# Performance work log

Measured on AMD Instinct MI355X. Metric: run time of the kernel, lower is better.

Reference implementation:

```python
import jax, jax.numpy as jnp
import numpy as np

N_NODES = 100000
N_EDGES = 3200000
IN_DIM = 128
HID = 64


def _gcn_conv(x, src, dst, norm, W, b, n_nodes):
    # x: [N, Fin]; PyG GCNConv: h = x @ W^T, propagate with sym norm, + bias
    h = x @ W.T                                  # [N, Fout]
    msg = h[src] * norm[:, None]                 # gather + scale, [E', Fout]
    out = jax.ops.segment_sum(msg, dst, num_segments=n_nodes)  # scatter-add
    return out + b


def _build_norm(edge_index, n_nodes):
    # add self-loops, compute D^-1/2 A D^-1/2 edge weights
    loops = jnp.arange(n_nodes, dtype=edge_index.dtype)
    src = jnp.concatenate([edge_index[0], loops])
    dst = jnp.concatenate([edge_index[1], loops])
    deg = jax.ops.segment_sum(jnp.ones_like(dst, dtype=jnp.float32), dst,
                              num_segments=n_nodes)
    dinv = jnp.where(deg > 0, jax.lax.rsqrt(jnp.maximum(deg, 1.0)), 0.0)
    norm = dinv[src] * dinv[dst]
    return src, dst, norm


def setup_inputs() -> dict:
    key = jax.random.key(0)
    k = jax.random.split(key, 8)
    x = jax.random.normal(k[0], (N_NODES, IN_DIM), dtype=jnp.float32)
    edge_index = jax.random.randint(k[1], (2, N_EDGES), 0, N_NODES, dtype=jnp.int64)
    s1 = 1.0 / np.sqrt(IN_DIM)
    s2 = 1.0 / np.sqrt(HID)
    W1 = jax.random.uniform(k[2], (HID, IN_DIM), jnp.float32, -s1, s1)
    b1 = jnp.zeros((HID,), jnp.float32)
    W2 = jax.random.uniform(k[3], (HID, HID), jnp.float32, -s2, s2)
    b2 = jnp.zeros((HID,), jnp.float32)
    Wc = jax.random.uniform(k[4], (1, HID), jnp.float32, -s2, s2)
    bc = jax.random.uniform(k[5], (1,), jnp.float32, -s2, s2)
    return {"x": x, "edge_index": edge_index, "W1": W1, "b1": b1,
            "W2": W2, "b2": b2, "Wc": Wc, "bc": bc}


def reference(x, edge_index, W1, b1, W2, b2, Wc, bc):
    n = x.shape[0]
    src, dst, norm = _build_norm(edge_index, n)
    h = _gcn_conv(x, src, dst, norm, W1, b1, n)
    h = jax.nn.relu(h)
    h = _gcn_conv(h, src, dst, norm, W2, b2, n)
    return h @ Wc.T + bc                          # [N, 1]
```

## Files before the change

### kernel.cpp

```cpp
#include <hip/hip_runtime.h>
#include <hip/hip_bf16.h>
#include <hip/hip_fp16.h>

#define N_NODES 100000
#define N_EDGES 3200000
#define F_IN    128
#define F_H     64

#define NBUCK 256
#define NPB   391
#define SRC_BITS 17

#define BH_T 256
#define BH_C 16384
__global__ __launch_bounds__(BH_T) void k_bhist(const int* __restrict__ dst,
                                                int* __restrict__ bcount) {
    __shared__ int lc[NBUCK];
    int t = threadIdx.x;
    lc[t] = 0;
    __syncthreads();
    long long e0 = (long long)blockIdx.x * BH_C;
    long long e1 = e0 + BH_C; if (e1 > N_EDGES) e1 = N_EDGES;
    for (long long e = e0 + t; e < e1; e += BH_T)
        atomicAdd(&lc[dst[e] / NPB], 1);
    __syncthreads();
    int c = lc[t];
    if (c) atomicAdd(&bcount[t], c);
}

__global__ __launch_bounds__(NBUCK) void k_bscan(const int* __restrict__ bcount,
                                                 int* __restrict__ bbase,
                                                 int* __restrict__ bcur,
                                                 int* __restrict__ row_ptr) {
    __shared__ int s[NBUCK];
    int t = threadIdx.x;
    int c = bcount[t];
    s[t] = c;
    __syncthreads();
    for (int off = 1; off < NBUCK; off <<= 1) {
        int v = (t >= off) ? s[t - off] : 0;
        __syncthreads();
        s[t] += v;
        __syncthreads();
    }
    int ex = s[t] - c;
    bbase[t] = ex;
    bcur[t]  = ex;
    if (t == NBUCK - 1) {
        bbase[NBUCK] = s[t];
        row_ptr[N_NODES] = s[t];
    }
}

__global__ __launch_bounds__(64) void k_wc2(const float* __restrict__ W2,
                                            const float* __restrict__ Wc,
                                            const float* __restrict__ b2,
                                            const float* __restrict__ bc,
                                            float* __restrict__ wc2,
                                            float* __restrict__ c0) {
    int k = threadIdx.x;
    float s = 0.0f;
#pragma unroll 8
    for (int f = 0; f < F_H; f++) s += Wc[f] * W2[f * F_H + k];
    wc2[k] = s;
    float p = Wc[k] * b2[k];
#pragma unroll
    for (int off = 32; off > 0; off >>= 1) p += __shfl_xor(p, off, 64);
    if (k == 0) c0[0] = p + bc[0];
}

#define PA_T   256
#define PA_C   4096
#define PA_PER (PA_C / PA_T)
__global__ __launch_bounds__(PA_T) void k_partA(const int* __restrict__ src,
                                                const int* __restrict__ dst,
                                                int* __restrict__ bucket_cursor,
                                                int* __restrict__ packT) {
    __shared__ int lcount[NBUCK];
    __shared__ int lstart[NBUCK];
    __shared__ int loffs[NBUCK];
    __shared__ int lbase[NBUCK];
    __shared__ int s_pack[PA_C];
    __shared__ unsigned char s_bkt[PA_C];
    __shared__ int ltot;
    int t = threadIdx.x;
    long long e0 = (long long)blockIdx.x * PA_C;
    if (t < NBUCK) lcount[t] = 0;
    __syncthreads();
    int ep[PA_PER];
    short eb[PA_PER];
#pragma unroll
    for (int i = 0; i < PA_PER; i++) {
        long long e = e0 + i * PA_T + t;
        if (e < N_EDGES) {
            int es = src[e], ed = dst[e];
            int b = ed / NPB;
            eb[i] = (short)b;
            ep[i] = ((ed - b * NPB) << SRC_BITS) | es;
            atomicAdd(&lcount[b], 1);
        } else eb[i] = -1;
    }
    __syncthreads();
    if (t < 64) {
        int base = t * 4;
        int c0 = lcount[base], c1 = lcount[base + 1], c2 = lcount[base + 2], c3 = lcount[base + 3];
        int ssum = c0 + c1 + c2 + c3;
        int sc = ssum;
#pragma unroll
        for (int off = 1; off < 64; off <<= 1) {
            int v = __shfl_up(sc, off, 64);
            if (t >= off) sc += v;
        }
        int ex = sc - ssum;
        lstart[base]     = ex;
        lstart[base + 1] = ex + c0;
        lstart[base + 2] = ex + c0 + c1;
        lstart[base + 3] = ex + c0 + c1 + c2;
        if (t == 63) ltot = sc;
    }
    __syncthreads();
    if (t < NBUCK) {
        loffs[t] = lstart[t];
        int c = lcount[t];
        lbase[t] = c ? atomicAdd(&bucket_cursor[t], c) : 0;
    }
    __syncthreads();
#pragma unroll
    for (int i = 0; i < PA_PER; i++) {
        if (eb[i] >= 0) {
            int idx = atomicAdd(&loffs[eb[i]], 1);
            s_pack[idx] = ep[i];
            s_bkt[idx] = (unsigned char)eb[i];
        }
    }
    __syncthreads();
    int tot = ltot;
    for (int i = t; i < tot; i += PA_T) {
        int b = s_bkt[i];
        int addr = lbase[b] + (i - lstart[b]);
        packT[addr] = s_pack[i];
    }
}

#define PB_T   1024
#define PB_CAP 16384
__global__ __launch_bounds__(PB_T) void k_partB(const int* __restrict__ bbase,
                                                const int* __restrict__ packT,
                                                int* __restrict__ row_ptr,
                                                float* __restrict__ dinv,
                                                int* __restrict__ srcs) {
    __shared__ int lhist[NPB];
    __shared__ int lcur[NPB];
    __shared__ int s_out[PB_CAP];
    int b = blockIdx.x;
    int node0 = b * NPB;
    int node1 = min(node0 + NPB, N_NODES);
    int nloc = node1 - node0;
    int beg = bbase[b];
    int end = bbase[b + 1];
    int len = end - beg;
    int t = threadIdx.x;
    const int SMASK = (1 << SRC_BITS) - 1;

    for (int i = t; i < NPB; i += PB_T) lhist[i] = 0;
    __syncthreads();
    for (int i = t; i < len; i += PB_T)
        atomicAdd(&lhist[packT[beg + i] >> SRC_BITS], 1);
    __syncthreads();
    if (t < 64) {
        int base = t * 7;
        int c[7]; int ssum = 0;
#pragma unroll
        for (int j = 0; j < 7; j++) {
            int idx = base + j;
            c[j] = (idx < NPB) ? lhist[idx] : 0;
            ssum += c[j];
        }
        int sc = ssum;
#pragma unroll
        for (int off = 1; off < 64; off <<= 1) {
            int v = __shfl_up(sc, off, 64);
            if (t >= off) sc += v;
        }
        int ex = sc - ssum;
#pragma unroll
        for (int j = 0; j < 7; j++) {
            int idx = base + j;
            if (idx < NPB) lcur[idx] = ex;
            ex += c[j];
        }
    }
    __syncthreads();
    for (int i = t; i < nloc; i += PB_T) {
        row_ptr[node0 + i] = beg + lcur[i];
        dinv[node0 + i] = rsqrtf((float)(lhist[i] + 1));
    }
    __syncthreads();
    if (len <= PB_CAP) {
        for (int i = t; i < len; i += PB_T) {
            int pk = packT[beg + i];
            int idx = atomicAdd(&lcur[pk >> SRC_BITS], 1);
            s_out[idx] = pk & SMASK;
        }
        __syncthreads();
        for (int i = t; i < len; i += PB_T)
            srcs[beg + i] = s_out[i];
    } else {
        for (int i = t; i < len; i += PB_T) {
            int pk = packT[beg + i];
            int idx = atomicAdd(&lcur[pk >> SRC_BITS], 1);
            srcs[beg + idx] = pk & SMASK;
        }
    }
}

#define GT   256
#define NTB  128
#define KT   64
#define WTS  68

__global__ __launch_bounds__(GT) void k_gemm1(const float* __restrict__ x,
                                              const float* __restrict__ W1,
                                              const float* __restrict__ dinv,
                                              __half* __restrict__ hs) {
    __shared__ float wT[KT * WTS];
    __shared__ float xT[KT * NTB];
    int t = threadIdx.x;
    int node0 = blockIdx.x * NTB;
    int lane = t & 63, wv = t >> 6;
    int fi = lane & 15, ni = lane >> 4;
    int n0 = wv * 32 + ni * 8;

    float acc[4][8];
#pragma unroll
    for (int r = 0; r < 4; r++)
#pragma unroll
        for (int c = 0; c < 8; c++) acc[r][c] = 0.0f;

    for (int p = 0; p < 2; p++) {
        int k0 = p * KT;
        if (p) __syncthreads();
        {
            int f = t & 63, kq = t >> 6;
            const float4* wp = (const float4*)&W1[(size_t)f * F_IN + k0 + kq * 16];
#pragma unroll
            for (int j = 0; j < 4; j++) {
                float4 v = wp[j];
                int kl = kq * 16 + 4 * j;
                wT[(kl + 0) * WTS + f] = v.x;
                wT[(kl + 1) * WTS + f] = v.y;
                wT[(kl + 2) * WTS + f] = v.z;
                wT[(kl + 3) * WTS + f] = v.w;
            }
        }
        {
            int n = t & 127, half = t >> 7;
            int node = node0 + n;
#pragma unroll
            for (int j = 0; j < 8; j++) {
                int ku = half * 8 + j;
                float4 v = make_float4(0.f, 0.f, 0.f, 0.f);
                if (node < N_NODES)
                    v = *(const float4*)&x[(size_t)node * F_IN + k0 + 4 * ku];
                int kl = 4 * ku;
                xT[(kl + 0) * NTB + n] = v.x;
                xT[(kl + 1) * NTB + n] = v.y;
                xT[(kl + 2) * NTB + n] = v.z;
                xT[(kl + 3) * NTB + n] = v.w;
            }
        }
        __syncthreads();
#pragma unroll 8
        for (int k = 0; k < KT; k++) {
            float4 wf = *(const float4*)&wT[k * WTS + fi * 4];
            float4 xa = *(const float4*)&xT[k * NTB + n0];
            float4 xb = *(const float4*)&xT[k * NTB + n0 + 4];
            float wr[4] = {wf.x, wf.y, wf.z, wf.w};
            float xv[8] = {xa.x, xa.y, xa.z, xa.w, xb.x, xb.y, xb.z, xb.w};
#pragma unroll
            for (int r = 0; r < 4; r++)
#pragma unroll
                for (int c = 0; c < 8; c++) acc[r][c] += wr[r] * xv[c];
        }
    }
#pragma unroll
    for (int c = 0; c < 8; c++) {
        int node = node0 + n0 + c;
        if (node < N_NODES) {
            float dv = dinv[node];
            __half2 h0 = __floats2half2_rn(acc[0][c] * dv, acc[1][c] * dv);
            __half2 h1 = __floats2half2_rn(acc[2][c] * dv, acc[3][c] * dv);
            __half2* p = (__half2*)&hs[(size_t)node * F_H + fi * 4];
            p[0] = h0; p[1] = h1;
        }
    }
}

__global__ void k_agg1q(const int* __restrict__ row_ptr, const int* __restrict__ srcs,
                        const __half* __restrict__ hs, const float* __restrict__ dinv,
                        const float* __restrict__ b1, const float* __restrict__ wc2,
                        float* __restrict__ q) {
    unsigned tid = blockIdx.x * blockDim.x + threadIdx.x;
    unsigned node = tid >> 6;
    int f = tid & 63;
    if (node >= N_NODES) return;
    int beg = row_ptr[node], end = row_ptr[node + 1];
    float v = __half2float(hs[(size_t)node * F_H + f]);
    int j = beg;
    for (; j + 8 <= end; j += 8) {
        int s0 = srcs[j],     s1 = srcs[j + 1], s2 = srcs[j + 2], s3 = srcs[j + 3];
        int s4 = srcs[j + 4], s5 = srcs[j + 5], s6 = srcs[j + 6], s7 = srcs[j + 7];
        float a0 = __half2float(hs[(size_t)s0 * F_H + f]);
        float a1 = __half2float(hs[(size_t)s1 * F_H + f]);
        float a2 = __half2float(hs[(size_t)s2 * F_H + f]);
        float a3 = __half2float(hs[(size_t)s3 * F_H + f]);
        float a4 = __half2float(hs[(size_t)s4 * F_H + f]);
        float a5 = __half2float(hs[(size_t)s5 * F_H + f]);
        float a6 = __half2float(hs[(size_t)s6 * F_H + f]);
        float a7 = __half2float(hs[(size_t)s7 * F_H + f]);
        v += ((a0 + a1) + (a2 + a3)) + ((a4 + a5) + (a6 + a7));
    }
    for (; j < end; j++) v += __half2float(hs[(size_t)srcs[j] * F_H + f]);
    float dv = dinv[node];
    float z = fmaxf(dv * v + b1[f], 0.0f);
    float p = z * wc2[f];
#pragma unroll
    for (int off = 32; off > 0; off >>= 1)
        p += __shfl_xor(p, off, 64);
    if (f == 0) q[node] = dv * p;
}

__global__ void k_final(const int* __restrict__ row_ptr, const int* __restrict__ srcs,
                        const float* __restrict__ q, const float* __restrict__ dinv,
                        const float* __restrict__ c0, float* __restrict__ out) {
    int node = blockIdx.x * blockDim.x + threadIdx.x;
    if (node >= N_NODES) return;
    int beg = row_ptr[node], end = row_ptr[node + 1];
    float acc = q[node];
    int j = beg;
    for (; j + 4 <= end; j += 4) {
        int s0 = srcs[j], s1 = srcs[j + 1], s2 = srcs[j + 2], s3 = srcs[j + 3];
        float a0 = q[s0], a1 = q[s1], a2 = q[s2], a3 = q[s3];
        acc += (a0 + a1) + (a2 + a3);
    }
    for (; j < end; j++) acc += q[srcs[j]];
    out[node] = dinv[node] * acc + c0[0];
}

extern "C" void kernel_launch(void* const* d_in, const int* in_sizes, int n_in,
                              void* d_out, int out_size, void* d_ws, size_t ws_size,
                              hipStream_t stream) {
    const float* x  = (const float*)d_in[0];
    const int*   ei = (const int*)d_in[1];
    const int*   src = ei;
    const int*   dst = ei + N_EDGES;
    const float* W1 = (const float*)d_in[2];
    const float* b1 = (const float*)d_in[3];
    const float* W2 = (const float*)d_in[4];
    const float* b2 = (const float*)d_in[5];
    const float* Wc = (const float*)d_in[6];
    const float* bc = (const float*)d_in[7];
    float* out = (float*)d_out;

    char* w = (char*)d_ws;
    int*    bcount  = (int*)w;    w += NBUCK * 4;
    int*    bbase   = (int*)w;    w += (NBUCK + 1) * 4;
    int*    bcur    = (int*)w;    w += NBUCK * 4;
    float*  wc2     = (float*)w;  w += 64 * 4;
    float*  c0      = (float*)w;  w += 4 * 4;
    int*    row_ptr = (int*)w;    w += ((size_t)N_NODES + 4) * 4;
    float*  dinv    = (float*)w;  w += (size_t)N_NODES * 4;
    float*  q       = (float*)w;  w += (size_t)N_NODES * 4;
    int*    srcs    = (int*)w;    w += (size_t)N_EDGES * 4;
    __half* bufA    = (__half*)w; w += (size_t)N_NODES * F_H * 2;
    int*    packT   = (int*)w;    w += (size_t)N_EDGES * 4;

    const int TB = 256;
    const int NB_BH = (int)(((long long)N_EDGES + BH_C - 1) / BH_C);
    const int NB_PA = (int)(((long long)N_EDGES + PA_C - 1) / PA_C);
    const int NB_G  = (N_NODES + NTB - 1) / NTB;

    hipMemsetAsync(bcount, 0, NBUCK * 4, stream);
    k_bhist<<<NB_BH, BH_T, 0, stream>>>(dst, bcount);
    k_bscan<<<1, NBUCK, 0, stream>>>(bcount, bbase, bcur, row_ptr);
    k_wc2  <<<1, 64, 0, stream>>>(W2, Wc, b2, bc, wc2, c0);
    k_partA<<<NB_PA, PA_T, 0, stream>>>(src, dst, bcur, packT);
    k_partB<<<NBUCK, PB_T, 0, stream>>>(bbase, packT, row_ptr, dinv, srcs);

    k_gemm1<<<NB_G, GT, 0, stream>>>(x, W1, dinv, bufA);
    k_agg1q<<<((unsigned)N_NODES * 64 + TB - 1) / TB, TB, 0, stream>>>(row_ptr, srcs, bufA, dinv, b1, wc2, q);

    k_final<<<(N_NODES + TB - 1) / TB, TB, 0, stream>>>(row_ptr, srcs, q, dinv, c0, out);
}
```

Before: 323.3 us.

## Replace CSR row gather with per-bucket shared-memory scatter-add aggregation

Drops the per-node CSR build. Edges are kept in destination buckets of 196 nodes, and within each bucket they are sorted by source range to improve gather locality on the half-precision features. Aggregation and the final layer each run one block per bucket and accumulate into a shared-memory tile with LDS float atomics. This removes the row-pointer construction and the per-node irregular loops. In exchange it adds shared-memory atomic contention, limits occupancy with a large LDS tile, and makes float summation order nondeterministic.

```diff
diff --git a/kernel.cpp b/kernel.cpp
--- a/kernel.cpp
+++ b/kernel.cpp
@@ -7,9 +7,10 @@
 #define F_IN    128
 #define F_H     64
 
-#define NBUCK 256
-#define NPB   391
+#define NBUCK 512
+#define NPB   196
 #define SRC_BITS 17
+#define SB    196
 
 #define BH_T 256
 #define BH_C 16384
@@ -17,21 +18,21 @@
                                                 int* __restrict__ bcount) {
     __shared__ int lc[NBUCK];
     int t = threadIdx.x;
-    lc[t] = 0;
+    lc[t] = 0; lc[t + 256] = 0;
     __syncthreads();
     long long e0 = (long long)blockIdx.x * BH_C;
     long long e1 = e0 + BH_C; if (e1 > N_EDGES) e1 = N_EDGES;
     for (long long e = e0 + t; e < e1; e += BH_T)
         atomicAdd(&lc[dst[e] / NPB], 1);
     __syncthreads();
-    int c = lc[t];
-    if (c) atomicAdd(&bcount[t], c);
+    int c0 = lc[t], c1 = lc[t + 256];
+    if (c0) atomicAdd(&bcount[t], c0);
+    if (c1) atomicAdd(&bcount[t + 256], c1);
 }
 
 __global__ __launch_bounds__(NBUCK) void k_bscan(const int* __restrict__ bcount,
                                                  int* __restrict__ bbase,
-                                                 int* __restrict__ bcur,
-                                                 int* __restrict__ row_ptr) {
+                                                 int* __restrict__ bcur) {
     __shared__ int s[NBUCK];
     int t = threadIdx.x;
     int c = bcount[t];
@@ -46,10 +47,7 @@
     int ex = s[t] - c;
     bbase[t] = ex;
     bcur[t]  = ex;
-    if (t == NBUCK - 1) {
-        bbase[NBUCK] = s[t];
-        row_ptr[N_NODES] = s[t];
-    }
+    if (t == NBUCK - 1) bbase[NBUCK] = s[t];
 }
 
 __global__ __launch_bounds__(64) void k_wc2(const float* __restrict__ W2,
@@ -81,11 +79,11 @@
     __shared__ int loffs[NBUCK];
     __shared__ int lbase[NBUCK];
     __shared__ int s_pack[PA_C];
-    __shared__ unsigned char s_bkt[PA_C];
+    __shared__ short s_bkt[PA_C];
     __shared__ int ltot;
     int t = threadIdx.x;
     long long e0 = (long long)blockIdx.x * PA_C;
-    if (t < NBUCK) lcount[t] = 0;
+    lcount[t] = 0; lcount[t + 256] = 0;
     __syncthreads();
     int ep[PA_PER];
     short eb[PA_PER];
@@ -102,9 +100,10 @@
     }
     __syncthreads();
     if (t < 64) {
-        int base = t * 4;
-        int c0 = lcount[base], c1 = lcount[base + 1], c2 = lcount[base + 2], c3 = lcount[base + 3];
-        int ssum = c0 + c1 + c2 + c3;
+        int base = t * 8;
+        int c[8]; int ssum = 0;
+#pragma unroll
+        for (int j = 0; j < 8; j++) { c[j] = lcount[base + j]; ssum += c[j]; }
         int sc = ssum;
 #pragma unroll
         for (int off = 1; off < 64; off <<= 1) {
@@ -112,17 +111,18 @@
             if (t >= off) sc += v;
         }
         int ex = sc - ssum;
-        lstart[base]     = ex;
-        lstart[base + 1] = ex + c0;
-        lstart[base + 2] = ex + c0 + c1;
-        lstart[base + 3] = ex + c0 + c1 + c2;
-        if (t == 63) ltot = sc;
-    }
-    __syncthreads();
-    if (t < NBUCK) {
-        loffs[t] = lstart[t];
-        int c = lcount[t];
-        lbase[t] = c ? atomicAdd(&bucket_cursor[t], c) : 0;
+#pragma unroll
+        for (int j = 0; j < 8; j++) { lstart[base + j] = ex; ex += c[j]; }
+        if (t == 63) ltot = ex;
+    }
+    __syncthreads();
+    {
+        int b0 = t, b1 = t + 256;
+        loffs[b0] = lstart[b0];
+        loffs[b1] = lstart[b1];
+        int c0 = lcount[b0], c1 = lcount[b1];
+        lbase[b0] = c0 ? atomicAdd(&bucket_cursor[b0], c0) : 0;
+        lbase[b1] = c1 ? atomicAdd(&bucket_cursor[b1], c1) : 0;
     }
     __syncthreads();
 #pragma unroll
@@ -130,7 +130,7 @@
         if (eb[i] >= 0) {
             int idx = atomicAdd(&loffs[eb[i]], 1);
             s_pack[idx] = ep[i];
-            s_bkt[idx] = (unsigned char)eb[i];
+            s_bkt[idx] = eb[i];
         }
     }
     __syncthreads();
@@ -142,38 +142,41 @@
     }
 }
 
-#define PB_T   1024
-#define PB_CAP 16384
+#define PB_T   512
+#define PB_CAP 8192
 __global__ __launch_bounds__(PB_T) void k_partB(const int* __restrict__ bbase,
                                                 const int* __restrict__ packT,
-                                                int* __restrict__ row_ptr,
                                                 float* __restrict__ dinv,
-                                                int* __restrict__ srcs) {
-    __shared__ int lhist[NPB];
-    __shared__ int lcur[NPB];
+                                                int* __restrict__ packS) {
+    __shared__ int lhd[NPB];
+    __shared__ int lhs[SB];
+    __shared__ int lcur[SB];
     __shared__ int s_out[PB_CAP];
     int b = blockIdx.x;
     int node0 = b * NPB;
-    int node1 = min(node0 + NPB, N_NODES);
-    int nloc = node1 - node0;
-    int beg = bbase[b];
-    int end = bbase[b + 1];
-    int len = end - beg;
+    int nloc = N_NODES - node0; if (nloc > NPB) nloc = NPB; if (nloc < 0) nloc = 0;
+    int beg = bbase[b], end = bbase[b + 1], len = end - beg;
     int t = threadIdx.x;
     const int SMASK = (1 << SRC_BITS) - 1;
 
-    for (int i = t; i < NPB; i += PB_T) lhist[i] = 0;
-    __syncthreads();
-    for (int i = t; i < len; i += PB_T)
-        atomicAdd(&lhist[packT[beg + i] >> SRC_BITS], 1);
-    __syncthreads();
+    for (int i = t; i < NPB; i += PB_T) lhd[i] = 0;
+    for (int i = t; i < SB; i += PB_T) lhs[i] = 0;
+    __syncthreads();
+    for (int i = t; i < len; i += PB_T) {
+        int pk = packT[beg + i];
+        atomicAdd(&lhd[pk >> SRC_BITS], 1);
+        atomicAdd(&lhs[(pk & SMASK) >> 9], 1);
+    }
+    __syncthreads();
+    for (int i = t; i < nloc; i += PB_T)
+        dinv[node0 + i] = rsqrtf((float)(lhd[i] + 1));
     if (t < 64) {
-        int base = t * 7;
-        int c[7]; int ssum = 0;
-#pragma unroll
-        for (int j = 0; j < 7; j++) {
+        int base = t * 4;
+        int c[4]; int ssum = 0;
+#pragma unroll
+        for (int j = 0; j < 4; j++) {
             int idx = base + j;
-            c[j] = (idx < NPB) ? lhist[idx] : 0;
+            c[j] = (idx < SB) ? lhs[idx] : 0;
             ssum += c[j];
         }
         int sc = ssum;
@@ -184,33 +187,25 @@
         }
         int ex = sc - ssum;
 #pragma unroll
-        for (int j = 0; j < 7; j++) {
+        for (int j = 0; j < 4; j++) {
             int idx = base + j;
-            if (idx < NPB) lcur[idx] = ex;
+            if (idx < SB) lcur[idx] = ex;
             ex += c[j];
         }
-    }
-    __syncthreads();
-    for (int i = t; i < nloc; i += PB_T) {
-        row_ptr[node0 + i] = beg + lcur[i];
-        dinv[node0 + i] = rsqrtf((float)(lhist[i] + 1));
     }
     __syncthreads();
     if (len <= PB_CAP) {
         for (int i = t; i < len; i += PB_T) {
             int pk = packT[beg + i];
-            int idx = atomicAdd(&lcur[pk >> SRC_BITS], 1);
-            s_out[idx] = pk & SMASK;
+            int idx = atomicAdd(&lcur[(pk & SMASK) >> 9], 1);
+            s_out[idx] = pk;
         }
         __syncthreads();
         for (int i = t; i < len; i += PB_T)
-            srcs[beg + i] = s_out[i];
+            packS[beg + i] = s_out[i];
     } else {
-        for (int i = t; i < len; i += PB_T) {
-            int pk = packT[beg + i];
-            int idx = atomicAdd(&lcur[pk >> SRC_BITS], 1);
-            srcs[beg + idx] = pk & SMASK;
-        }
+        for (int i = t; i < len; i += PB_T)
+            packS[beg + i] = packT[beg + i];
     }
 }
 
@@ -296,55 +291,95 @@
     }
 }
 
-__global__ void k_agg1q(const int* __restrict__ row_ptr, const int* __restrict__ srcs,
-                        const __half* __restrict__ hs, const float* __restrict__ dinv,
-                        const float* __restrict__ b1, const float* __restrict__ wc2,
-                        float* __restrict__ q) {
-    unsigned tid = blockIdx.x * blockDim.x + threadIdx.x;
-    unsigned node = tid >> 6;
-    int f = tid & 63;
-    if (node >= N_NODES) return;
-    int beg = row_ptr[node], end = row_ptr[node + 1];
-    float v = __half2float(hs[(size_t)node * F_H + f]);
-    int j = beg;
-    for (; j + 8 <= end; j += 8) {
-        int s0 = srcs[j],     s1 = srcs[j + 1], s2 = srcs[j + 2], s3 = srcs[j + 3];
-        int s4 = srcs[j + 4], s5 = srcs[j + 5], s6 = srcs[j + 6], s7 = srcs[j + 7];
-        float a0 = __half2float(hs[(size_t)s0 * F_H + f]);
-        float a1 = __half2float(hs[(size_t)s1 * F_H + f]);
-        float a2 = __half2float(hs[(size_t)s2 * F_H + f]);
-        float a3 = __half2float(hs[(size_t)s3 * F_H + f]);
-        float a4 = __half2float(hs[(size_t)s4 * F_H + f]);
-        float a5 = __half2float(hs[(size_t)s5 * F_H + f]);
-        float a6 = __half2float(hs[(size_t)s6 * F_H + f]);
-        float a7 = __half2float(hs[(size_t)s7 * F_H + f]);
-        v += ((a0 + a1) + (a2 + a3)) + ((a4 + a5) + (a6 + a7));
-    }
-    for (; j < end; j++) v += __half2float(hs[(size_t)srcs[j] * F_H + f]);
-    float dv = dinv[node];
-    float z = fmaxf(dv * v + b1[f], 0.0f);
-    float p = z * wc2[f];
-#pragma unroll
-    for (int off = 32; off > 0; off >>= 1)
-        p += __shfl_xor(p, off, 64);
-    if (f == 0) q[node] = dv * p;
-}
-
-__global__ void k_final(const int* __restrict__ row_ptr, const int* __restrict__ srcs,
-                        const float* __restrict__ q, const float* __restrict__ dinv,
-                        const float* __restrict__ c0, float* __restrict__ out) {
-    int node = blockIdx.x * blockDim.x + threadIdx.x;
-    if (node >= N_NODES) return;
-    int beg = row_ptr[node], end = row_ptr[node + 1];
-    float acc = q[node];
-    int j = beg;
-    for (; j + 4 <= end; j += 4) {
-        int s0 = srcs[j], s1 = srcs[j + 1], s2 = srcs[j + 2], s3 = srcs[j + 3];
-        float a0 = q[s0], a1 = q[s1], a2 = q[s2], a3 = q[s3];
-        acc += (a0 + a1) + (a2 + a3);
-    }
-    for (; j < end; j++) acc += q[srcs[j]];
-    out[node] = dinv[node] * acc + c0[0];
+#define AG_T 512
+#define AG_W (AG_T / 64)
+__global__ __launch_bounds__(AG_T) void k_agg1(const int* __restrict__ bbase,
+                                               const int* __restrict__ packS,
+                                               const __half* __restrict__ hs,
+                                               const float* __restrict__ dinv,
+                                               const float* __restrict__ b1,
+                                               const float* __restrict__ wc2,
+                                               float* __restrict__ q) {
+    __shared__ float acc[NPB * F_H];
+    int b = blockIdx.x;
+    int node0 = b * NPB;
+    int nloc = N_NODES - node0; if (nloc > NPB) nloc = NPB; if (nloc < 0) nloc = 0;
+    int t = threadIdx.x, lane = t & 63, wv = t >> 6;
+    const int SMASK = (1 << SRC_BITS) - 1;
+
+    for (int i = wv; i < nloc; i += AG_W)
+        acc[i * F_H + lane] = __half2float(hs[(size_t)(node0 + i) * F_H + lane]);
+    __syncthreads();
+
+    int beg = bbase[b], len = bbase[b + 1] - beg;
+    for (int blk = wv; blk * 8 < len; blk += AG_W) {
+        int e0 = beg + blk * 8;
+        int n8 = len - blk * 8; if (n8 > 8) n8 = 8;
+        if (n8 == 8) {
+            int pk0 = packS[e0 + 0], pk1 = packS[e0 + 1];
+            int pk2 = packS[e0 + 2], pk3 = packS[e0 + 3];
+            int pk4 = packS[e0 + 4], pk5 = packS[e0 + 5];
+            int pk6 = packS[e0 + 6], pk7 = packS[e0 + 7];
+            float v0 = __half2float(hs[(size_t)(pk0 & SMASK) * F_H + lane]);
+            float v1 = __half2float(hs[(size_t)(pk1 & SMASK) * F_H + lane]);
+            float v2 = __half2float(hs[(size_t)(pk2 & SMASK) * F_H + lane]);
+            float v3 = __half2float(hs[(size_t)(pk3 & SMASK) * F_H + lane]);
+            float v4 = __half2float(hs[(size_t)(pk4 & SMASK) * F_H + lane]);
+            float v5 = __half2float(hs[(size_t)(pk5 & SMASK) * F_H + lane]);
+            float v6 = __half2float(hs[(size_t)(pk6 & SMASK) * F_H + lane]);
+            float v7 = __half2float(hs[(size_t)(pk7 & SMASK) * F_H + lane]);
+            atomicAdd(&acc[(pk0 >> SRC_BITS) * F_H + lane], v0);
+            atomicAdd(&acc[(pk1 >> SRC_BITS) * F_H + lane], v1);
+            atomicAdd(&acc[(pk2 >> SRC_BITS) * F_H + lane], v2);
+            atomicAdd(&acc[(pk3 >> SRC_BITS) * F_H + lane], v3);
+            atomicAdd(&acc[(pk4 >> SRC_BITS) * F_H + lane], v4);
+            atomicAdd(&acc[(pk5 >> SRC_BITS) * F_H + lane], v5);
+            atomicAdd(&acc[(pk6 >> SRC_BITS) * F_H + lane], v6);
+            atomicAdd(&acc[(pk7 >> SRC_BITS) * F_H + lane], v7);
+        } else {
+            for (int j = 0; j < n8; j++) {
+                int pk = packS[e0 + j];
+                float v = __half2float(hs[(size_t)(pk & SMASK) * F_H + lane]);
+                atomicAdd(&acc[(pk >> SRC_BITS) * F_H + lane], v);
+            }
+        }
+    }
+    __syncthreads();
+    float bl = b1[lane], wl = wc2[lane];
+    for (int i = wv; i < nloc; i += AG_W) {
+        float dv = dinv[node0 + i];
+        float z = fmaxf(dv * acc[i * F_H + lane] + bl, 0.0f);
+        float p = z * wl;
+#pragma unroll
+        for (int off = 32; off > 0; off >>= 1)
+            p += __shfl_xor(p, off, 64);
+        if (lane == 0) q[node0 + i] = dv * p;
+    }
+}
+
+#define FN_T 256
+__global__ __launch_bounds__(FN_T) void k_final(const int* __restrict__ bbase,
+                                                const int* __restrict__ packS,
+                                                const float* __restrict__ q,
+                                                const float* __restrict__ dinv,
+                                                const float* __restrict__ c0,
+                                                float* __restrict__ out) {
+    __shared__ float sacc[NPB];
+    int b = blockIdx.x;
+    int node0 = b * NPB;
+    int nloc = N_NODES - node0; if (nloc > NPB) nloc = NPB; if (nloc < 0) nloc = 0;
+    int t = threadIdx.x;
+    const int SMASK = (1 << SRC_BITS) - 1;
+    for (int i = t; i < nloc; i += FN_T) sacc[i] = q[node0 + i];
+    __syncthreads();
+    int beg = bbase[b], len = bbase[b + 1] - beg;
+    for (int i = t; i < len; i += FN_T) {
+        int pk = packS[beg + i];
+        atomicAdd(&sacc[pk >> SRC_BITS], q[pk & SMASK]);
+    }
+    __syncthreads();
+    for (int i = t; i < nloc; i += FN_T)
+        out[node0 + i] = dinv[node0 + i] * sacc[i] + c0[0];
 }
 
 extern "C" void kernel_launch(void* const* d_in, const int* in_sizes, int n_in,
@@ -368,27 +403,25 @@
     int*    bcur    = (int*)w;    w += NBUCK * 4;
     float*  wc2     = (float*)w;  w += 64 * 4;
     float*  c0      = (float*)w;  w += 4 * 4;
-    int*    row_ptr = (int*)w;    w += ((size_t)N_NODES + 4) * 4;
     float*  dinv    = (float*)w;  w += (size_t)N_NODES * 4;
     float*  q       = (float*)w;  w += (size_t)N_NODES * 4;
-    int*    srcs    = (int*)w;    w += (size_t)N_EDGES * 4;
+    int*    packS   = (int*)w;    w += (size_t)N_EDGES * 4;
     __half* bufA    = (__half*)w; w += (size_t)N_NODES * F_H * 2;
     int*    packT   = (int*)w;    w += (size_t)N_EDGES * 4;
 
-    const int TB = 256;
     const int NB_BH = (int)(((long long)N_EDGES + BH_C - 1) / BH_C);
     const int NB_PA = (int)(((long long)N_EDGES + PA_C - 1) / PA_C);
     const int NB_G  = (N_NODES + NTB - 1) / NTB;
 
     hipMemsetAsync(bcount, 0, NBUCK * 4, stream);
     k_bhist<<<NB_BH, BH_T, 0, stream>>>(dst, bcount);
-    k_bscan<<<1, NBUCK, 0, stream>>>(bcount, bbase, bcur, row_ptr);
+    k_bscan<<<1, NBUCK, 0, stream>>>(bcount, bbase, bcur);
     k_wc2  <<<1, 64, 0, stream>>>(W2, Wc, b2, bc, wc2, c0);
     k_partA<<<NB_PA, PA_T, 0, stream>>>(src, dst, bcur, packT);
-    k_partB<<<NBUCK, PB_T, 0, stream>>>(bbase, packT, row_ptr, dinv, srcs);
+    k_partB<<<NBUCK, PB_T, 0, stream>>>(bbase, packT, dinv, packS);
 
     k_gemm1<<<NB_G, GT, 0, stream>>>(x, W1, dinv, bufA);
-    k_agg1q<<<((unsigned)N_NODES * 64 + TB - 1) / TB, TB, 0, stream>>>(row_ptr, srcs, bufA, dinv, b1, wc2, q);
-
-    k_final<<<(N_NODES + TB - 1) / TB, TB, 0, stream>>>(row_ptr, srcs, q, dinv, c0, out);
-}
+    k_agg1<<<NBUCK, AG_T, 0, stream>>>(bbase, packS, bufA, dinv, b1, wc2, q);
+
+    k_final<<<NBUCK, FN_T, 0, stream>>>(bbase, packS, q, dinv, c0, out);
+}
```

New measurement: 1.284 ms. 297% more time.
